# Kernel tuning notes

Measured on AMD Instinct MI355X. Metric: run time of the kernel, lower is better.

Reference implementation:

```python
import jax, jax.numpy as jnp
import numpy as np

ALPHA = float(np.exp(-0.1))  # leak factor exp(-dt/tau) with dt/tau = 0.1


def setup_inputs() -> dict:
    key = jax.random.key(0)
    k1, k2 = jax.random.split(key)
    B, T, H, O = 128, 512, 1024, 256
    x = jax.random.normal(k1, (B, T, H), dtype=jnp.float32)
    # xavier_uniform init for (H, O) weight
    limit = float(np.sqrt(6.0 / (H + O)))
    weight_end = jax.random.uniform(k2, (H, O), dtype=jnp.float32,
                                    minval=-limit, maxval=limit)
    return {"x": x, "weight_end": weight_end}


def reference(x, weight_end):
    # x: [B, T, H], weight_end: [H, O]
    h2 = jnp.einsum('bth,ho->bto', x, weight_end)  # [B, T, O]
    B, T, O = h2.shape
    # leaky-integrate scan over first T-1 steps, accumulating softmax(mem)
    h_seq = jnp.swapaxes(h2[:, :T - 1, :], 0, 1)  # [T-1, B, O]

    def step(carry, h_t):
        mem, out = carry
        mem = ALPHA * mem + (1.0 - ALPHA) * h_t
        out = out + jax.nn.softmax(mem, axis=-1)
        return (mem, out), None

    init = (jnp.zeros((B, O), h2.dtype), jnp.zeros((B, O), h2.dtype))
    (_, out), _ = jax.lax.scan(step, init, h_seq)
    return out
```

## Files before the change

### kernel.cpp

```cpp
#include <hip/hip_runtime.h>

#define B_DIM 128
#define T_DIM 512
#define H_DIM 1024
#define O_DIM 256

typedef short bf16x8 __attribute__((ext_vector_type(8)));
typedef float f32x4 __attribute__((ext_vector_type(4)));

__device__ __forceinline__ unsigned short f2bf(float f) {
    union { float f; unsigned u; } v; v.f = f;
    unsigned u = v.u;
    u += 0x7fffu + ((u >> 16) & 1u);
    return (unsigned short)(u >> 16);
}

__device__ __forceinline__ unsigned tpk(float a, float b) {
    union { float f; unsigned u; } x{a}, y{b};
    return __builtin_amdgcn_perm(y.u, x.u, 0x07060302u);
}

__device__ __forceinline__ void async16(const void* g, void* l) {
    __builtin_amdgcn_global_load_lds(
        (const __attribute__((address_space(1))) unsigned int*)g,
        (__attribute__((address_space(3))) unsigned int*)l, 16, 0, 0);
}

__global__ __launch_bounds__(256) void transpose_w(const float* __restrict__ W,
                                                   unsigned short* __restrict__ Wt) {
    __shared__ float tile[32][33];
    int h0 = blockIdx.x * 32;
    int o0 = blockIdx.y * 32;
    int tx = threadIdx.x;
    int ty = threadIdx.y;
#pragma unroll
    for (int j = 0; j < 32; j += 8)
        tile[ty + j][tx] = W[(size_t)(h0 + ty + j) * O_DIM + o0 + tx];
    __syncthreads();
    int h = h0 + tx;
#pragma unroll
    for (int j = 0; j < 32; j += 8) {
        int o = o0 + ty + j;
        size_t idx = (size_t)(o >> 7) * 131072 + (size_t)(h >> 5) * 4096 +
                     (size_t)((h >> 3) & 3) * 1024 + (size_t)(o & 127) * 8 + (h & 7);
        Wt[idx] = f2bf(tile[tx][ty + j]);
    }
}

__global__ __launch_bounds__(512, 4) void gemm_bf16(const float* __restrict__ x,
                                                    const unsigned short* __restrict__ Wtt,
                                                    unsigned short* __restrict__ h2) {
    __shared__ __align__(16) unsigned short As[2][128 * 40];
    __shared__ __align__(16) unsigned short Bs[2][8192];

    const int tid  = threadIdx.x;
    const int mb   = blockIdx.x;
    const int m0   = mb * 128;
    const int lane = tid & 63;
    const int wave = tid >> 6;
    const int wm   = wave >> 2, wn = wave & 3;
    const int rowsel = lane & 15, quad = lane >> 4;

    const int arow = tid >> 3;
    const int akf  = (tid & 7) * 4;
    const float* ag = x + (size_t)(m0 + arow) * H_DIM + akf;
    const int aoff = arow * 40 + akf;

    const unsigned short* bg0 = Wtt + (size_t)tid * 8;
    const unsigned short* bg1 = Wtt + 131072 + (size_t)tid * 8;

    f32x4 acc[4][4];
#pragma unroll
    for (int i = 0; i < 4; ++i)
#pragma unroll
        for (int j = 0; j < 4; ++j)
            acc[i][j] = (f32x4){0.f, 0.f, 0.f, 0.f};

    {
        float4 a0 = *(const float4*)(ag);
        float4 a1 = *(const float4*)(ag + (size_t)64 * H_DIM);
        unsigned short* bl = &Bs[0][tid * 8];
        async16(bg0, bl);
        async16(bg1, bl + 4096);
        uint2 p0, p1;
        p0.x = tpk(a0.x, a0.y); p0.y = tpk(a0.z, a0.w);
        p1.x = tpk(a1.x, a1.y); p1.y = tpk(a1.z, a1.w);
        *(uint2*)&As[0][aoff] = p0;
        *(uint2*)&As[0][aoff + 64 * 40] = p1;
    }

    const int nbsel = wn >> 1;
    const int bbase = nbsel * 4096 + quad * 1024;
    const int bcol0 = (wn & 1) * 64 + rowsel;

    for (int k = 0; k < 32; ++k) {
        const int cur = k & 1, nxt = cur ^ 1;
        __syncthreads();

        float4 a0, a1;
        if (k + 1 < 32) {
            const float* agk = ag + (size_t)(k + 1) * 32;
            a0 = *(const float4*)(agk);
            a1 = *(const float4*)(agk + (size_t)64 * H_DIM);
            const size_t bko = (size_t)(k + 1) * 4096;
            unsigned short* bl = &Bs[nxt][tid * 8];
            async16(bg0 + bko, bl);
            async16(bg1 + bko, bl + 4096);
        }

        bf16x8 af[4], bfr[4];
#pragma unroll
        for (int i = 0; i < 4; ++i) {
            af[i]  = *(const bf16x8*)&As[cur][(wm * 64 + rowsel + i * 16) * 40 + quad * 8];
            bfr[i] = *(const bf16x8*)&Bs[cur][bbase + (bcol0 + i * 16) * 8];
        }
#pragma unroll
        for (int i = 0; i < 4; ++i)
#pragma unroll
            for (int j = 0; j < 4; ++j)
                acc[i][j] = __builtin_amdgcn_mfma_f32_16x16x32_bf16(af[i], bfr[j], acc[i][j], 0, 0, 0);

        if (k + 1 < 32) {
            uint2 p0, p1;
            p0.x = tpk(a0.x, a0.y); p0.y = tpk(a0.z, a0.w);
            p1.x = tpk(a1.x, a1.y); p1.y = tpk(a1.z, a1.w);
            *(uint2*)&As[nxt][aoff] = p0;
            *(uint2*)&As[nxt][aoff + 64 * 40] = p1;
        }
    }

#pragma unroll
    for (int i = 0; i < 4; ++i) {
#pragma unroll
        for (int j = 0; j < 4; ++j) {
            int gm = m0 + wm * 64 + i * 16 + quad * 4;
            int gn = wn * 64 + j * 16 + rowsel;
            unsigned short* cp = h2 + (size_t)gm * O_DIM + gn;
            cp[0 * O_DIM] = f2bf(acc[i][j][0]);
            cp[1 * O_DIM] = f2bf(acc[i][j][1]);
            cp[2 * O_DIM] = f2bf(acc[i][j][2]);
            cp[3 * O_DIM] = f2bf(acc[i][j][3]);
        }
    }
}

__global__ __launch_bounds__(64) void snn_scan(const unsigned short* __restrict__ h2,
                                               float* __restrict__ out) {
    const int b = blockIdx.x >> 3;
    const int c = blockIdx.x & 7;
    const int t_start = c * 64;
    const int t_end   = min(t_start + 64, T_DIM - 1);
    const int s0      = max(0, t_start - 64);
    const int lane    = threadIdx.x;

    const float A   = 0.90483741803595957f;
    const float OMA = 0.09516258196404043f;

    const unsigned short* base = h2 + (size_t)b * T_DIM * O_DIM + lane * 4;
#define LD(row) (*(const uint2*)(base + (size_t)(row) * O_DIM))

    float4 mem = {0.f, 0.f, 0.f, 0.f};
    float4 acc = {0.f, 0.f, 0.f, 0.f};

    uint2 u0 = LD(s0), u1 = LD(s0 + 1), u2 = LD(s0 + 2), u3 = LD(s0 + 3);

    const int nIter = (t_end - s0 + 3) & ~3;

#define STEP(U, T)                                                              \
    {                                                                           \
        union { unsigned u; float f; } l0, h0, l1, h1;                          \
        l0.u = (U).x << 16; h0.u = (U).x & 0xffff0000u;                         \
        l1.u = (U).y << 16; h1.u = (U).y & 0xffff0000u;                         \
        mem.x = A * mem.x + OMA * l0.f;                                         \
        mem.y = A * mem.y + OMA * h0.f;                                         \
        mem.z = A * mem.z + OMA * l1.f;                                         \
        mem.w = A * mem.w + OMA * h1.f;                                         \
        if ((T) >= t_start && (T) < t_end) {                                    \
            float e0 = __expf(mem.x), e1 = __expf(mem.y);                       \
            float e2 = __expf(mem.z), e3 = __expf(mem.w);                       \
            float s = e0 + e1 + e2 + e3;                                        \
            s += __shfl_xor(s, 1);                                              \
            s += __shfl_xor(s, 2);                                              \
            s += __shfl_xor(s, 4);                                              \
            s += __shfl_xor(s, 8);                                              \
            s += __shfl_xor(s, 16);                                             \
            s += __shfl_xor(s, 32);                                             \
            float inv = 1.0f / s;                                               \
            acc.x += e0 * inv; acc.y += e1 * inv;                               \
            acc.z += e2 * inv; acc.w += e3 * inv;                               \
        }                                                                       \
    }

    for (int t = s0; t < s0 + nIter; t += 4) {
        STEP(u0, t);     u0 = LD(min(t + 4, T_DIM - 1));
        STEP(u1, t + 1); u1 = LD(min(t + 5, T_DIM - 1));
        STEP(u2, t + 2); u2 = LD(min(t + 6, T_DIM - 1));
        STEP(u3, t + 3); u3 = LD(min(t + 7, T_DIM - 1));
    }
#undef STEP
#undef LD

    float* op = out + b * O_DIM + lane * 4;
    atomicAdd(op + 0, acc.x);
    atomicAdd(op + 1, acc.y);
    atomicAdd(op + 2, acc.z);
    atomicAdd(op + 3, acc.w);
}

extern "C" void kernel_launch(void* const* d_in, const int* in_sizes, int n_in,
                              void* d_out, int out_size, void* d_ws, size_t ws_size,
                              hipStream_t stream) {
    const float* x = (const float*)d_in[0];
    const float* W = (const float*)d_in[1];
    float* out = (float*)d_out;

    unsigned short* h2 = (unsigned short*)d_ws;
    unsigned short* Wt = (unsigned short*)((char*)d_ws +
                         (size_t)B_DIM * T_DIM * O_DIM * sizeof(unsigned short));

    hipMemsetAsync(d_out, 0, (size_t)B_DIM * O_DIM * sizeof(float), stream);
    transpose_w<<<dim3(H_DIM / 32, O_DIM / 32), dim3(32, 8), 0, stream>>>(W, Wt);
    gemm_bf16<<<dim3(B_DIM * T_DIM / 128), 512, 0, stream>>>(x, Wt, h2);
    snn_scan<<<dim3(B_DIM * 8), 64, 0, stream>>>(h2, out);
}
```

Before: 433.5 us.

## Triple-buffer GEMM tiles with deeper prefetch and fold output zeroing into transpose

The GEMM moves from double to triple LDS buffering. B tiles are now loaded one stage ahead and A tiles two stages ahead in registers, with explicit vmcnt/lgkmcnt waits, scheduling barriers and a single s_barrier per iteration. This lets global loads overlap more MFMA work and removes one barrier per iteration. The output memset is also folded into the transpose kernel, dropping a separate launch. In exchange, LDS use rises (about 55KB per block), which may limit occupancy against the launch_bounds target of 4 blocks.

```diff
diff --git a/kernel.cpp b/kernel.cpp
--- a/kernel.cpp
+++ b/kernel.cpp
@@ -26,9 +26,19 @@
         (__attribute__((address_space(3))) unsigned int*)l, 16, 0, 0);
 }
 
+#define SB() __builtin_amdgcn_sched_barrier(0)
+
 __global__ __launch_bounds__(256) void transpose_w(const float* __restrict__ W,
-                                                   unsigned short* __restrict__ Wt) {
+                                                   unsigned short* __restrict__ Wt,
+                                                   float* __restrict__ out) {
     __shared__ float tile[32][33];
+    if (blockIdx.x == 0) {
+        int t = blockIdx.y * 256 + threadIdx.y * 32 + threadIdx.x;
+        float4 z = {0.f, 0.f, 0.f, 0.f};
+        float4* o4 = (float4*)out;
+#pragma unroll
+        for (int i = 0; i < 4; ++i) o4[t * 4 + i] = z;
+    }
     int h0 = blockIdx.x * 32;
     int o0 = blockIdx.y * 32;
     int tx = threadIdx.x;
@@ -50,8 +60,8 @@
 __global__ __launch_bounds__(512, 4) void gemm_bf16(const float* __restrict__ x,
                                                     const unsigned short* __restrict__ Wtt,
                                                     unsigned short* __restrict__ h2) {
-    __shared__ __align__(16) unsigned short As[2][128 * 40];
-    __shared__ __align__(16) unsigned short Bs[2][8192];
+    __shared__ __align__(16) unsigned short As[3][128 * 40];
+    __shared__ __align__(16) unsigned short Bs[3][8192];
 
     const int tid  = threadIdx.x;
     const int mb   = blockIdx.x;
@@ -76,37 +86,44 @@
         for (int j = 0; j < 4; ++j)
             acc[i][j] = (f32x4){0.f, 0.f, 0.f, 0.f};
 
-    {
-        float4 a0 = *(const float4*)(ag);
-        float4 a1 = *(const float4*)(ag + (size_t)64 * H_DIM);
-        unsigned short* bl = &Bs[0][tid * 8];
-        async16(bg0, bl);
-        async16(bg1, bl + 4096);
-        uint2 p0, p1;
-        p0.x = tpk(a0.x, a0.y); p0.y = tpk(a0.z, a0.w);
-        p1.x = tpk(a1.x, a1.y); p1.y = tpk(a1.z, a1.w);
-        *(uint2*)&As[0][aoff] = p0;
-        *(uint2*)&As[0][aoff + 64 * 40] = p1;
-    }
-
     const int nbsel = wn >> 1;
     const int bbase = nbsel * 4096 + quad * 1024;
     const int bcol0 = (wn & 1) * 64 + rowsel;
 
-    for (int k = 0; k < 32; ++k) {
-        const int cur = k & 1, nxt = cur ^ 1;
-        __syncthreads();
-
-        float4 a0, a1;
-        if (k + 1 < 32) {
-            const float* agk = ag + (size_t)(k + 1) * 32;
-            a0 = *(const float4*)(agk);
-            a1 = *(const float4*)(agk + (size_t)64 * H_DIM);
-            const size_t bko = (size_t)(k + 1) * 4096;
-            unsigned short* bl = &Bs[nxt][tid * 8];
-            async16(bg0 + bko, bl);
-            async16(bg1 + bko, bl + 4096);
-        }
+    float4 aX0, aX1;
+
+    {
+        float4 t0 = *(const float4*)(ag);
+        float4 t1 = *(const float4*)(ag + (size_t)64 * H_DIM);
+        SB();
+        async16(bg0, &Bs[0][tid * 8]);
+        async16(bg1, &Bs[0][tid * 8 + 4096]);
+        SB();
+        aX0 = *(const float4*)(ag + 32);
+        aX1 = *(const float4*)(ag + 32 + (size_t)64 * H_DIM);
+        SB();
+        uint2 p0, p1;
+        p0.x = tpk(t0.x, t0.y); p0.y = tpk(t0.z, t0.w);
+        p1.x = tpk(t1.x, t1.y); p1.y = tpk(t1.z, t1.w);
+        *(uint2*)&As[0][aoff] = p0;
+        *(uint2*)&As[0][aoff + 64 * 40] = p1;
+        asm volatile("s_waitcnt vmcnt(2)" ::: "memory");
+        asm volatile("s_waitcnt lgkmcnt(0)" ::: "memory");
+        __builtin_amdgcn_s_barrier();
+        SB();
+    }
+
+    for (int k = 0; k < 30; ++k) {
+        const int cur = k % 3, nxt = (k + 1) % 3;
+
+        const size_t bko = (size_t)(k + 1) * 4096;
+        async16(bg0 + bko, &Bs[nxt][tid * 8]);
+        async16(bg1 + bko, &Bs[nxt][tid * 8 + 4096]);
+        SB();
+        const float* agk = ag + (size_t)(k + 2) * 32;
+        float4 t0 = *(const float4*)(agk);
+        float4 t1 = *(const float4*)(agk + (size_t)64 * H_DIM);
+        SB();
 
         bf16x8 af[4], bfr[4];
 #pragma unroll
@@ -120,13 +137,63 @@
             for (int j = 0; j < 4; ++j)
                 acc[i][j] = __builtin_amdgcn_mfma_f32_16x16x32_bf16(af[i], bfr[j], acc[i][j], 0, 0, 0);
 
-        if (k + 1 < 32) {
+        {
             uint2 p0, p1;
-            p0.x = tpk(a0.x, a0.y); p0.y = tpk(a0.z, a0.w);
-            p1.x = tpk(a1.x, a1.y); p1.y = tpk(a1.z, a1.w);
+            p0.x = tpk(aX0.x, aX0.y); p0.y = tpk(aX0.z, aX0.w);
+            p1.x = tpk(aX1.x, aX1.y); p1.y = tpk(aX1.z, aX1.w);
             *(uint2*)&As[nxt][aoff] = p0;
             *(uint2*)&As[nxt][aoff + 64 * 40] = p1;
         }
+        aX0 = t0; aX1 = t1;
+
+        asm volatile("s_waitcnt vmcnt(2)" ::: "memory");
+        asm volatile("s_waitcnt lgkmcnt(0)" ::: "memory");
+        __builtin_amdgcn_s_barrier();
+        SB();
+    }
+
+    {
+        const size_t bko = (size_t)31 * 4096;
+        async16(bg0 + bko, &Bs[1][tid * 8]);
+        async16(bg1 + bko, &Bs[1][tid * 8 + 4096]);
+        SB();
+
+        bf16x8 af[4], bfr[4];
+#pragma unroll
+        for (int i = 0; i < 4; ++i) {
+            af[i]  = *(const bf16x8*)&As[0][(wm * 64 + rowsel + i * 16) * 40 + quad * 8];
+            bfr[i] = *(const bf16x8*)&Bs[0][bbase + (bcol0 + i * 16) * 8];
+        }
+#pragma unroll
+        for (int i = 0; i < 4; ++i)
+#pragma unroll
+            for (int j = 0; j < 4; ++j)
+                acc[i][j] = __builtin_amdgcn_mfma_f32_16x16x32_bf16(af[i], bfr[j], acc[i][j], 0, 0, 0);
+
+        uint2 p0, p1;
+        p0.x = tpk(aX0.x, aX0.y); p0.y = tpk(aX0.z, aX0.w);
+        p1.x = tpk(aX1.x, aX1.y); p1.y = tpk(aX1.z, aX1.w);
+        *(uint2*)&As[1][aoff] = p0;
+        *(uint2*)&As[1][aoff + 64 * 40] = p1;
+
+        asm volatile("s_waitcnt vmcnt(0)" ::: "memory");
+        asm volatile("s_waitcnt lgkmcnt(0)" ::: "memory");
+        __builtin_amdgcn_s_barrier();
+        SB();
+    }
+
+    {
+        bf16x8 af[4], bfr[4];
+#pragma unroll
+        for (int i = 0; i < 4; ++i) {
+            af[i]  = *(const bf16x8*)&As[1][(wm * 64 + rowsel + i * 16) * 40 + quad * 8];
+            bfr[i] = *(const bf16x8*)&Bs[1][bbase + (bcol0 + i * 16) * 8];
+        }
+#pragma unroll
+        for (int i = 0; i < 4; ++i)
+#pragma unroll
+            for (int j = 0; j < 4; ++j)
+                acc[i][j] = __builtin_amdgcn_mfma_f32_16x16x32_bf16(af[i], bfr[j], acc[i][j], 0, 0, 0);
     }
 
 #pragma unroll
@@ -218,8 +285,7 @@
     unsigned short* Wt = (unsigned short*)((char*)d_ws +
                          (size_t)B_DIM * T_DIM * O_DIM * sizeof(unsigned short));
 
-    hipMemsetAsync(d_out, 0, (size_t)B_DIM * O_DIM * sizeof(float), stream);
-    transpose_w<<<dim3(H_DIM / 32, O_DIM / 32), dim3(32, 8), 0, stream>>>(W, Wt);
+    transpose_w<<<dim3(H_DIM / 32, O_DIM / 32), dim3(32, 8), 0, stream>>>(W, Wt, out);
     gemm_bf16<<<dim3(B_DIM * T_DIM / 128), 512, 0, stream>>>(x, Wt, h2);
     snn_scan<<<dim3(B_DIM * 8), 64, 0, stream>>>(h2, out);
 }
```

Measured after the change: 430.8 us. About the same (-0.6%).
